# Kernel tuning notes

Measured on AMD Instinct MI355X. Metric: run time of the kernel, lower is better.

## Reference

```python
import jax, jax.numpy as jnp
import numpy as np

B, C, E = 2, 1024, 1024
H = 16            # n_heads as declared (used as per-group feature dim due to module's reshape)
HD = E // H       # 64 — the axis actually batched over in attention


def setup_inputs() -> dict:
    key = jax.random.key(0)
    ks = jax.random.split(key, 5)
    scale = 0.02
    return {
        "x": jax.random.normal(ks[0], (B, C, E), dtype=jnp.float32),
        "W_q": jax.random.normal(ks[1], (E, E), dtype=jnp.float32) * scale,
        "W_k": jax.random.normal(ks[2], (E, E), dtype=jnp.float32) * scale,
        "W_v": jax.random.normal(ks[3], (E, E), dtype=jnp.float32) * scale,
        "W_o": jax.random.normal(ks[4], (E, E), dtype=jnp.float32) * scale,
    }


def reference(x, W_q, W_k, W_v, W_o):
    # nn.Linear: y = x @ W.T  (bias=False)
    def proj_split(W):
        y = jnp.einsum('bce,de->bcd', x, W)              # [B,C,E]
        # view(B, C, HD, H).transpose(1,2) -> [B, HD, C, H]  (faithful to source layout)
        return y.reshape(B, C, HD, H).transpose(0, 2, 1, 3)

    Q = proj_split(W_q)
    K = proj_split(W_k)
    V = proj_split(W_v)

    scale = 1.0 / jnp.sqrt(jnp.asarray(H, dtype=x.dtype))  # sqrt of last dim (= n_heads here)
    scores = jnp.einsum('bdqh,bdkh->bdqk', Q, K) * scale    # [B, HD, C, C]
    weights = jax.nn.softmax(scores, axis=-1)
    out = jnp.einsum('bdqk,bdkh->bdqh', weights, V)         # [B, HD, C, H]
    out = out.transpose(0, 2, 1, 3).reshape(B, C, E)        # [B, C, E]
    out = jnp.einsum('bce,de->bcd', out, W_o)
    return out  # dropout p=0.0 / eval mode: identity
```

## Files before the change

kernel.cpp:

```cpp
#include <hip/hip_runtime.h>
#include <stdint.h>
#include <math.h>


typedef __bf16   bf16x8 __attribute__((ext_vector_type(8)));
typedef float    f32x4  __attribute__((ext_vector_type(4)));

__device__ __forceinline__ unsigned short f2bf(float f) {
    unsigned int u = __float_as_uint(f);
    u += 0x7FFFu + ((u >> 16) & 1u);
    return (unsigned short)(u >> 16);
}

__device__ __forceinline__ unsigned int cvtpk(float lo, float hi) {
    unsigned int r;
    asm("v_cvt_pk_bf16_f32 %0, %1, %2" : "=v"(r) : "v"(lo), "v"(hi));
    return r;
}

__device__ __forceinline__ void gl16(const unsigned short* g, unsigned short* l) {
    __builtin_amdgcn_global_load_lds(
        (const __attribute__((address_space(1))) unsigned int*)g,
        (__attribute__((address_space(3))) unsigned int*)l, 16, 0, 0);
}

__global__ __launch_bounds__(256) void cast_to_bf16(
    const float* __restrict__ x,
    const float* __restrict__ w0, const float* __restrict__ w1,
    const float* __restrict__ w2, const float* __restrict__ w3,
    unsigned short* __restrict__ xb,
    unsigned short* __restrict__ b0, unsigned short* __restrict__ b1,
    unsigned short* __restrict__ b2, unsigned short* __restrict__ b3)
{
    const int z = blockIdx.y;
    const float* src;
    unsigned short* dst;
    size_t off = 0;
    float sc = 1.f;
    if (z < 2)       { src = x;  dst = xb; off = (size_t)z << 20; }
    else if (z == 2) { src = w0; dst = b0; sc = 0.36067376022224085f; }
    else if (z == 3) { src = w1; dst = b1; }
    else if (z == 4) { src = w2; dst = b2; }
    else             { src = w3; dst = b3; }
    const size_t i = off + ((size_t)blockIdx.x * 256 + threadIdx.x) * 4;
    const float4 v = *(const float4*)(src + i);
    *(ushort4*)(dst + i) = make_ushort4(f2bf(v.x * sc), f2bf(v.y * sc),
                                        f2bf(v.z * sc), f2bf(v.w * sc));
}

__global__ __launch_bounds__(256) void gemm128_bt_mfma(
    const unsigned short* __restrict__ A,
    const unsigned short* __restrict__ B0, const unsigned short* __restrict__ B1,
    const unsigned short* __restrict__ B2,
    unsigned short* __restrict__ C0, unsigned short* __restrict__ C1,
    unsigned short* __restrict__ C2,
    int M, int N, int K)
{
    const unsigned short* Bm = (blockIdx.z == 0) ? B0 : (blockIdx.z == 1) ? B1 : B2;
    unsigned short* Cm       = (blockIdx.z == 0) ? C0 : (blockIdx.z == 1) ? C1 : C2;

    __shared__ __align__(16) unsigned short As[2][128 * 32];
    __shared__ __align__(16) unsigned short Bs[2][128 * 32];

    const int t    = threadIdx.x;
    const int lane = t & 63;
    const int w    = t >> 6;
    const int m0   = blockIdx.y * 128;
    const int n0   = blockIdx.x * 128;
    const int wm   = (w & 1) * 64;
    const int wn   = (w >> 1) * 64;

    const int r0 = t >> 2;
    const int c0 = (t & 3) * 8;
    const unsigned short* Apa = A  + (size_t)(m0 + r0) * K + c0;
    const unsigned short* Apb = Apa + (size_t)64 * K;
    const unsigned short* Bpa = Bm + (size_t)(n0 + r0) * K + c0;
    const unsigned short* Bpb = Bpa + (size_t)64 * K;
    unsigned short* lA0 = &As[0][w * 512];
    unsigned short* lA1 = &As[0][2048 + w * 512];
    unsigned short* lB0 = &Bs[0][w * 512];
    unsigned short* lB1 = &Bs[0][2048 + w * 512];
    const int bufStr = 128 * 32;

    f32x4 acc[4][4];
#pragma unroll
    for (int i = 0; i < 4; ++i)
#pragma unroll
        for (int j = 0; j < 4; ++j) acc[i][j] = (f32x4){0.f, 0.f, 0.f, 0.f};

    const int fm = lane & 15;
    const int kg = lane >> 4;

    gl16(Apa, lA0);
    gl16(Apb, lA1);
    gl16(Bpa, lB0);
    gl16(Bpb, lB1);

    int cur = 0;
    for (int k0 = 0; k0 < K; k0 += 32) {
        __syncthreads();

        if (k0 + 32 < K) {
            const int nb = (cur ^ 1);
            gl16(Apa + k0 + 32, lA0 + nb * bufStr);
            gl16(Apb + k0 + 32, lA1 + nb * bufStr);
            gl16(Bpa + k0 + 32, lB0 + nb * bufStr);
            gl16(Bpb + k0 + 32, lB1 + nb * bufStr);
        }

        const unsigned short* Ab = &As[cur][0];
        const unsigned short* Bb = &Bs[cur][0];
        bf16x8 af[4], bfr[4];
#pragma unroll
        for (int im = 0; im < 4; ++im)
            af[im] = *(const bf16x8*)&Ab[(wm + im * 16 + fm) * 32 + kg * 8];
#pragma unroll
        for (int in = 0; in < 4; ++in)
            bfr[in] = *(const bf16x8*)&Bb[(wn + in * 16 + fm) * 32 + kg * 8];
#pragma unroll
        for (int im = 0; im < 4; ++im)
#pragma unroll
            for (int in = 0; in < 4; ++in)
                acc[im][in] = __builtin_amdgcn_mfma_f32_16x16x32_bf16(
                    af[im], bfr[in], acc[im][in], 0, 0, 0);

        cur ^= 1;
    }

#pragma unroll
    for (int im = 0; im < 4; ++im) {
#pragma unroll
        for (int in = 0; in < 4; ++in) {
            const int row = m0 + wm + im * 16 + kg * 4;
            const int col = n0 + wn + in * 16 + fm;
#pragma unroll
            for (int r = 0; r < 4; ++r)
                Cm[(size_t)(row + r) * N + col] = f2bf(acc[im][in][r]);
        }
    }
}

__global__ __launch_bounds__(256) void gemm_bt_mfma(
    const unsigned short* __restrict__ A,
    const unsigned short* __restrict__ B0, const unsigned short* __restrict__ B1,
    const unsigned short* __restrict__ B2,
    void* __restrict__ C0, void* __restrict__ C1, void* __restrict__ C2,
    int M, int N, int K, int bf16out)
{
    const unsigned short* Bm = (blockIdx.z == 0) ? B0 : (blockIdx.z == 1) ? B1 : B2;
    void* Cm                 = (blockIdx.z == 0) ? C0 : (blockIdx.z == 1) ? C1 : C2;

    __shared__ __align__(16) unsigned short As[2][64 * 32];
    __shared__ __align__(16) unsigned short Bs[2][128 * 32];

    const int t    = threadIdx.x;
    const int lane = t & 63;
    const int w    = t >> 6;
    const int m0   = blockIdx.y * 64;
    const int n0   = blockIdx.x * 128;
    const int wm   = (w & 1) * 32;
    const int wn   = (w >> 1) * 64;

    const int r0 = t >> 2;
    const int c0 = (t & 3) * 8;
    const unsigned short* Apa = A  + (size_t)(m0 + r0) * K + c0;
    const unsigned short* Bpa = Bm + (size_t)(n0 + r0) * K + c0;
    const unsigned short* Bpb = Bm + (size_t)(n0 + r0 + 64) * K + c0;
    unsigned short* ldsA  = &As[0][w * 512];
    unsigned short* ldsB0 = &Bs[0][w * 512];
    unsigned short* ldsB1 = &Bs[0][2048 + w * 512];
    const int bufStrA = 64 * 32;
    const int bufStrB = 128 * 32;

    f32x4 acc[2][4];
#pragma unroll
    for (int i = 0; i < 2; ++i)
#pragma unroll
        for (int j = 0; j < 4; ++j) acc[i][j] = (f32x4){0.f, 0.f, 0.f, 0.f};

    const int fm = lane & 15;
    const int kg = lane >> 4;

    gl16(Apa, ldsA);
    gl16(Bpa, ldsB0);
    gl16(Bpb, ldsB1);

    int cur = 0;
    for (int k0 = 0; k0 < K; k0 += 32) {
        __syncthreads();

        if (k0 + 32 < K) {
            const int nb = (cur ^ 1);
            gl16(Apa + k0 + 32, ldsA  + nb * bufStrA);
            gl16(Bpa + k0 + 32, ldsB0 + nb * bufStrB);
            gl16(Bpb + k0 + 32, ldsB1 + nb * bufStrB);
        }

        const unsigned short* Ab = &As[cur][0];
        const unsigned short* Bb = &Bs[cur][0];
        bf16x8 af[2], bfr[4];
#pragma unroll
        for (int im = 0; im < 2; ++im)
            af[im] = *(const bf16x8*)&Ab[(wm + im * 16 + fm) * 32 + kg * 8];
#pragma unroll
        for (int in = 0; in < 4; ++in)
            bfr[in] = *(const bf16x8*)&Bb[(wn + in * 16 + fm) * 32 + kg * 8];
#pragma unroll
        for (int im = 0; im < 2; ++im)
#pragma unroll
            for (int in = 0; in < 4; ++in)
                acc[im][in] = __builtin_amdgcn_mfma_f32_16x16x32_bf16(
                    af[im], bfr[in], acc[im][in], 0, 0, 0);

        cur ^= 1;
    }

#pragma unroll
    for (int im = 0; im < 2; ++im) {
#pragma unroll
        for (int in = 0; in < 4; ++in) {
            const int row = m0 + wm + im * 16 + kg * 4;
            const int col = n0 + wn + in * 16 + fm;
            if (bf16out) {
                unsigned short* cp = (unsigned short*)Cm;
#pragma unroll
                for (int r = 0; r < 4; ++r)
                    cp[(size_t)(row + r) * N + col] = f2bf(acc[im][in][r]);
            } else {
                float* cp = (float*)Cm;
#pragma unroll
                for (int r = 0; r < 4; ++r)
                    cp[(size_t)(row + r) * N + col] = acc[im][in][r];
            }
        }
    }
}

#define KSTR  40
#define VSTRD 136
#define PSTRD 136

__global__ __launch_bounds__(256, 3) void attn_mfma(
    const unsigned short* __restrict__ Qb, const unsigned short* __restrict__ Kb,
    const unsigned short* __restrict__ Vb, unsigned short* __restrict__ Ob)
{
    __shared__ __align__(16) unsigned char smem[49408];
    unsigned short* Ks  = (unsigned short*)smem;
    unsigned short* VsT = (unsigned short*)(smem + 10240);
    unsigned short* Ps  = (unsigned short*)(smem + 14592);
    float*          Red = (float*)smem;

    const int t    = threadIdx.x;
    const int lane = t & 63;
    const int wv   = t >> 6;
    const int fm   = lane & 15;
    const int kg   = lane >> 4;
    const int bh   = blockIdx.y;
    const size_t base = ((size_t)(bh >> 6) << 20) + (size_t)(bh & 63) * 16;
    const int q0 = blockIdx.x * 128;
    const int wk = wv * 32;

    {
        const int row = t >> 1, seg = t & 1;
        *(uint4*)&Ks[row * KSTR + 16 + seg * 8] = make_uint4(0, 0, 0, 0);
    }

    union { uint4 u; bf16x8 h; } zz; zz.u = make_uint4(0, 0, 0, 0);
    bf16x8 aq[8];
#pragma unroll
    for (int m = 0; m < 8; ++m) {
        if (kg < 2)
            aq[m] = *(const bf16x8*)(Qb + base +
                     (size_t)(q0 + m * 16 + fm) * 1024 + kg * 8);
        else
            aq[m] = zz.h;
    }

    f32x4 oacc[8];
    float lp[8];
#pragma unroll
    for (int m = 0; m < 8; ++m) {
        oacc[m] = (f32x4){0.f, 0.f, 0.f, 0.f};
        lp[m] = 0.f;
    }

    for (int kt = 0; kt < 1024; kt += 128) {
        __syncthreads();
        {
            const int row = t >> 1, seg = t & 1;
            *(uint4*)&Ks[row * KSTR + seg * 8] =
                *(const uint4*)(Kb + base + (size_t)(kt + row) * 1024 + seg * 8);
            uint4 v = *(const uint4*)(Vb + base + (size_t)(kt + row) * 1024 + seg * 8);
            const unsigned short* pv = (const unsigned short*)&v;
#pragma unroll
            for (int d = 0; d < 8; ++d)
                VsT[(seg * 8 + d) * VSTRD + row] = pv[d];
        }
        __syncthreads();

        const bf16x8 bk0 = *(const bf16x8*)&Ks[(wk + fm) * KSTR + kg * 8];
        const bf16x8 bk1 = *(const bf16x8*)&Ks[(wk + 16 + fm) * KSTR + kg * 8];

#pragma unroll
        for (int m = 0; m < 8; ++m) {
            f32x4 s0 = __builtin_amdgcn_mfma_f32_16x16x32_bf16(
                bk0, aq[m], (f32x4){0.f, 0.f, 0.f, 0.f}, 0, 0, 0);
            f32x4 s1 = __builtin_amdgcn_mfma_f32_16x16x32_bf16(
                bk1, aq[m], (f32x4){0.f, 0.f, 0.f, 0.f}, 0, 0, 0);
            const float p0 = __builtin_amdgcn_exp2f(s0[0]);
            const float p1 = __builtin_amdgcn_exp2f(s0[1]);
            const float p2 = __builtin_amdgcn_exp2f(s0[2]);
            const float p3 = __builtin_amdgcn_exp2f(s0[3]);
            const float p4 = __builtin_amdgcn_exp2f(s1[0]);
            const float p5 = __builtin_amdgcn_exp2f(s1[1]);
            const float p6 = __builtin_amdgcn_exp2f(s1[2]);
            const float p7 = __builtin_amdgcn_exp2f(s1[3]);
            lp[m] += ((p0 + p1) + (p2 + p3)) + ((p4 + p5) + (p6 + p7));
            unsigned short* prow = &Ps[(m * 16 + fm) * PSTRD + wk];
            *(uint2*)&prow[kg * 4]      = make_uint2(cvtpk(p0, p1), cvtpk(p2, p3));
            *(uint2*)&prow[16 + kg * 4] = make_uint2(cvtpk(p4, p5), cvtpk(p6, p7));
        }

        const bf16x8 bv = *(const bf16x8*)&VsT[fm * VSTRD + wk + kg * 8];
#pragma unroll
        for (int m = 0; m < 8; ++m) {
            const bf16x8 ap = *(const bf16x8*)&Ps[(m * 16 + fm) * PSTRD + wk + kg * 8];
            oacc[m] = __builtin_amdgcn_mfma_f32_16x16x32_bf16(ap, bv, oacc[m], 0, 0, 0);
        }
    }

#pragma unroll
    for (int m = 0; m < 8; ++m) {
        lp[m] += __shfl_xor(lp[m], 16, 64);
        lp[m] += __shfl_xor(lp[m], 32, 64);
    }

    __syncthreads();
#pragma unroll
    for (int m = 0; m < 8; ++m) {
#pragma unroll
        for (int r = 0; r < 4; ++r)
            Red[((wv * 128) + m * 16 + kg * 4 + r) * 17 + fm] = oacc[m][r];
        if (kg == 0)
            Red[((wv * 128) + m * 16 + fm) * 17 + 16] = lp[m];
    }
    __syncthreads();

#pragma unroll
    for (int mp = 0; mp < 2; ++mp) {
#pragma unroll
        for (int r = 0; r < 4; ++r) {
            const int q = wv * 32 + mp * 16 + kg * 4 + r;
            const float o = Red[q * 17 + fm]         + Red[(128 + q) * 17 + fm] +
                            Red[(256 + q) * 17 + fm] + Red[(384 + q) * 17 + fm];
            const float l = Red[q * 17 + 16]         + Red[(128 + q) * 17 + 16] +
                            Red[(256 + q) * 17 + 16] + Red[(384 + q) * 17 + 16];
            Ob[base + (size_t)(q0 + q) * 1024 + fm] = f2bf(o / l);
        }
    }
}

extern "C" void kernel_launch(void* const* d_in, const int* in_sizes, int n_in,
                              void* d_out, int out_size, void* d_ws, size_t ws_size,
                              hipStream_t stream) {
    const float* x  = (const float*)d_in[0];
    const float* Wq = (const float*)d_in[1];
    const float* Wk = (const float*)d_in[2];
    const float* Wv = (const float*)d_in[3];
    const float* Wo = (const float*)d_in[4];
    float* out = (float*)d_out;

    const int M = 2048, N = 1024, Kd = 1024;
    const size_t MEG = 1048576;
    unsigned short* ws = (unsigned short*)d_ws;
    unsigned short* xb  = ws;
    unsigned short* Wqb = ws + 2 * MEG;
    unsigned short* Wkb = ws + 3 * MEG;
    unsigned short* Wvb = ws + 4 * MEG;
    unsigned short* Wob = ws + 5 * MEG;
    unsigned short* Qb  = ws + 6 * MEG;
    unsigned short* Kb  = ws + 8 * MEG;
    unsigned short* Vb  = ws + 10 * MEG;
    unsigned short* Ob  = ws + 12 * MEG;

    dim3 gc(1024, 6, 1);
    cast_to_bf16<<<gc, 256, 0, stream>>>(x, Wq, Wk, Wv, Wo, xb, Wqb, Wkb, Wvb, Wob);

    dim3 g1(N / 128, M / 128, 3);
    gemm128_bt_mfma<<<g1, 256, 0, stream>>>(xb, Wqb, Wkb, Wvb, Qb, Kb, Vb, M, N, Kd);

    dim3 g2(8, 128, 1);
    attn_mfma<<<g2, 256, 0, stream>>>(Qb, Kb, Vb, Ob);

    dim3 g3(N / 128, M / 64, 1);
    gemm_bt_mfma<<<g3, 256, 0, stream>>>(Ob, Wob, Wob, Wob, out, out, out, M, N, Kd, 0);
}
```

Measured before the change: 153.3 us.

## Fuse all stages into one persistent kernel with atomic grid barriers

Replaces the four separate launches (cast, QKV GEMM, attention, output GEMM) with a single persistent kernel of 512 blocks. Each block loops over the work tiles of every stage, and a spin-wait atomic grid barrier separates the stages. The aim is to remove launch gaps and inter-kernel drain/fill overhead. In exchange, the attention stage drops from occupancy 3 to launch bounds of 2, and tiles are distributed unevenly per block (384 and 256 tiles over 512 blocks leave some idle). A memset is added to reset the barrier counters, and correctness depends on all 512 blocks being co-resident.

After: 298.3 us. +94.6%, slower.

```diff
diff --git a/kernel.cpp b/kernel.cpp
--- a/kernel.cpp
+++ b/kernel.cpp
@@ -5,6 +5,8 @@
 
 typedef __bf16   bf16x8 __attribute__((ext_vector_type(8)));
 typedef float    f32x4  __attribute__((ext_vector_type(4)));
+
+#define NBLK 512
 
 __device__ __forceinline__ unsigned short f2bf(float f) {
     unsigned int u = __float_as_uint(f);
@@ -24,49 +26,36 @@
         (__attribute__((address_space(3))) unsigned int*)l, 16, 0, 0);
 }
 
-__global__ __launch_bounds__(256) void cast_to_bf16(
-    const float* __restrict__ x,
-    const float* __restrict__ w0, const float* __restrict__ w1,
-    const float* __restrict__ w2, const float* __restrict__ w3,
-    unsigned short* __restrict__ xb,
-    unsigned short* __restrict__ b0, unsigned short* __restrict__ b1,
-    unsigned short* __restrict__ b2, unsigned short* __restrict__ b3)
+__device__ __forceinline__ void gridbar(unsigned int* cnt) {
+    __syncthreads();
+    if (threadIdx.x == 0) {
+        __threadfence();
+        atomicAdd(cnt, 1u);
+        while (__hip_atomic_load(cnt, __ATOMIC_RELAXED,
+                                 __HIP_MEMORY_SCOPE_AGENT) < NBLK)
+            __builtin_amdgcn_s_sleep(4);
+        __threadfence();
+    }
+    __syncthreads();
+}
+
+__device__ void dev_gemm128(int bx, int by, int bz, unsigned char* smem,
+    const unsigned short* A,
+    const unsigned short* B0, const unsigned short* B1, const unsigned short* B2,
+    unsigned short* C0, unsigned short* C1, unsigned short* C2)
 {
-    const int z = blockIdx.y;
-    const float* src;
-    unsigned short* dst;
-    size_t off = 0;
-    float sc = 1.f;
-    if (z < 2)       { src = x;  dst = xb; off = (size_t)z << 20; }
-    else if (z == 2) { src = w0; dst = b0; sc = 0.36067376022224085f; }
-    else if (z == 3) { src = w1; dst = b1; }
-    else if (z == 4) { src = w2; dst = b2; }
-    else             { src = w3; dst = b3; }
-    const size_t i = off + ((size_t)blockIdx.x * 256 + threadIdx.x) * 4;
-    const float4 v = *(const float4*)(src + i);
-    *(ushort4*)(dst + i) = make_ushort4(f2bf(v.x * sc), f2bf(v.y * sc),
-                                        f2bf(v.z * sc), f2bf(v.w * sc));
-}
-
-__global__ __launch_bounds__(256) void gemm128_bt_mfma(
-    const unsigned short* __restrict__ A,
-    const unsigned short* __restrict__ B0, const unsigned short* __restrict__ B1,
-    const unsigned short* __restrict__ B2,
-    unsigned short* __restrict__ C0, unsigned short* __restrict__ C1,
-    unsigned short* __restrict__ C2,
-    int M, int N, int K)
-{
-    const unsigned short* Bm = (blockIdx.z == 0) ? B0 : (blockIdx.z == 1) ? B1 : B2;
-    unsigned short* Cm       = (blockIdx.z == 0) ? C0 : (blockIdx.z == 1) ? C1 : C2;
-
-    __shared__ __align__(16) unsigned short As[2][128 * 32];
-    __shared__ __align__(16) unsigned short Bs[2][128 * 32];
+    const int K = 1024, N = 1024;
+    const unsigned short* Bm = (bz == 0) ? B0 : (bz == 1) ? B1 : B2;
+    unsigned short* Cm       = (bz == 0) ? C0 : (bz == 1) ? C1 : C2;
+
+    unsigned short* As = (unsigned short*)smem;
+    unsigned short* Bs = (unsigned short*)(smem + 16384);
 
     const int t    = threadIdx.x;
     const int lane = t & 63;
     const int w    = t >> 6;
-    const int m0   = blockIdx.y * 128;
-    const int n0   = blockIdx.x * 128;
+    const int m0   = by * 128;
+    const int n0   = bx * 128;
     const int wm   = (w & 1) * 64;
     const int wn   = (w >> 1) * 64;
 
@@ -76,10 +65,10 @@
     const unsigned short* Apb = Apa + (size_t)64 * K;
     const unsigned short* Bpa = Bm + (size_t)(n0 + r0) * K + c0;
     const unsigned short* Bpb = Bpa + (size_t)64 * K;
-    unsigned short* lA0 = &As[0][w * 512];
-    unsigned short* lA1 = &As[0][2048 + w * 512];
-    unsigned short* lB0 = &Bs[0][w * 512];
-    unsigned short* lB1 = &Bs[0][2048 + w * 512];
+    unsigned short* lA0 = As + w * 512;
+    unsigned short* lA1 = As + 2048 + w * 512;
+    unsigned short* lB0 = Bs + w * 512;
+    unsigned short* lB1 = Bs + 2048 + w * 512;
     const int bufStr = 128 * 32;
 
     f32x4 acc[4][4];
@@ -108,8 +97,8 @@
             gl16(Bpb + k0 + 32, lB1 + nb * bufStr);
         }
 
-        const unsigned short* Ab = &As[cur][0];
-        const unsigned short* Bb = &Bs[cur][0];
+        const unsigned short* Ab = As + cur * bufStr;
+        const unsigned short* Bb = Bs + cur * bufStr;
         bf16x8 af[4], bfr[4];
 #pragma unroll
         for (int im = 0; im < 4; ++im)
@@ -140,24 +129,18 @@
     }
 }
 
-__global__ __launch_bounds__(256) void gemm_bt_mfma(
-    const unsigned short* __restrict__ A,
-    const unsigned short* __restrict__ B0, const unsigned short* __restrict__ B1,
-    const unsigned short* __restrict__ B2,
-    void* __restrict__ C0, void* __restrict__ C1, void* __restrict__ C2,
-    int M, int N, int K, int bf16out)
+__device__ void dev_gemm64(int bx, int by, unsigned char* smem,
+    const unsigned short* A, const unsigned short* Bm, float* Cm)
 {
-    const unsigned short* Bm = (blockIdx.z == 0) ? B0 : (blockIdx.z == 1) ? B1 : B2;
-    void* Cm                 = (blockIdx.z == 0) ? C0 : (blockIdx.z == 1) ? C1 : C2;
-
-    __shared__ __align__(16) unsigned short As[2][64 * 32];
-    __shared__ __align__(16) unsigned short Bs[2][128 * 32];
+    const int K = 1024, N = 1024;
+    unsigned short* As = (unsigned short*)smem;
+    unsigned short* Bs = (unsigned short*)(smem + 8192);
 
     const int t    = threadIdx.x;
     const int lane = t & 63;
     const int w    = t >> 6;
-    const int m0   = blockIdx.y * 64;
-    const int n0   = blockIdx.x * 128;
+    const int m0   = by * 64;
+    const int n0   = bx * 128;
     const int wm   = (w & 1) * 32;
     const int wn   = (w >> 1) * 64;
 
@@ -166,9 +149,9 @@
     const unsigned short* Apa = A  + (size_t)(m0 + r0) * K + c0;
     const unsigned short* Bpa = Bm + (size_t)(n0 + r0) * K + c0;
     const unsigned short* Bpb = Bm + (size_t)(n0 + r0 + 64) * K + c0;
-    unsigned short* ldsA  = &As[0][w * 512];
-    unsigned short* ldsB0 = &Bs[0][w * 512];
-    unsigned short* ldsB1 = &Bs[0][2048 + w * 512];
+    unsigned short* ldsA  = As + w * 512;
+    unsigned short* ldsB0 = Bs + w * 512;
+    unsigned short* ldsB1 = Bs + 2048 + w * 512;
     const int bufStrA = 64 * 32;
     const int bufStrB = 128 * 32;
 
@@ -196,8 +179,8 @@
             gl16(Bpb + k0 + 32, ldsB1 + nb * bufStrB);
         }
 
-        const unsigned short* Ab = &As[cur][0];
-        const unsigned short* Bb = &Bs[cur][0];
+        const unsigned short* Ab = As + cur * bufStrA;
+        const unsigned short* Bb = Bs + cur * bufStrB;
         bf16x8 af[2], bfr[4];
 #pragma unroll
         for (int im = 0; im < 2; ++im)
@@ -221,17 +204,9 @@
         for (int in = 0; in < 4; ++in) {
             const int row = m0 + wm + im * 16 + kg * 4;
             const int col = n0 + wn + in * 16 + fm;
-            if (bf16out) {
-                unsigned short* cp = (unsigned short*)Cm;
-#pragma unroll
-                for (int r = 0; r < 4; ++r)
-                    cp[(size_t)(row + r) * N + col] = f2bf(acc[im][in][r]);
-            } else {
-                float* cp = (float*)Cm;
-#pragma unroll
-                for (int r = 0; r < 4; ++r)
-                    cp[(size_t)(row + r) * N + col] = acc[im][in][r];
-            }
+#pragma unroll
+            for (int r = 0; r < 4; ++r)
+                Cm[(size_t)(row + r) * N + col] = acc[im][in][r];
         }
     }
 }
@@ -240,11 +215,10 @@
 #define VSTRD 136
 #define PSTRD 136
 
-__global__ __launch_bounds__(256, 3) void attn_mfma(
-    const unsigned short* __restrict__ Qb, const unsigned short* __restrict__ Kb,
-    const unsigned short* __restrict__ Vb, unsigned short* __restrict__ Ob)
+__device__ void dev_attn(int bx, int by, unsigned char* smem,
+    const unsigned short* Qb, const unsigned short* Kb,
+    const unsigned short* Vb, unsigned short* Ob)
 {
-    __shared__ __align__(16) unsigned char smem[49408];
     unsigned short* Ks  = (unsigned short*)smem;
     unsigned short* VsT = (unsigned short*)(smem + 10240);
     unsigned short* Ps  = (unsigned short*)(smem + 14592);
@@ -255,10 +229,11 @@
     const int wv   = t >> 6;
     const int fm   = lane & 15;
     const int kg   = lane >> 4;
-    const int bh   = blockIdx.y;
-    const size_t base = ((size_t)(bh >> 6) << 20) + (size_t)(bh & 63) * 16;
-    const int q0 = blockIdx.x * 128;
+    const size_t base = ((size_t)(by >> 6) << 20) + (size_t)(by & 63) * 16;
+    const int q0 = bx * 128;
     const int wk = wv * 32;
+
+    __syncthreads();
 
     {
         const int row = t >> 1, seg = t & 1;
@@ -360,6 +335,58 @@
     }
 }
 
+__global__ __launch_bounds__(256, 2) void fused_mha(
+    const float* __restrict__ x,
+    const float* __restrict__ Wq, const float* __restrict__ Wk,
+    const float* __restrict__ Wv, const float* __restrict__ Wo,
+    unsigned short* ws16, float* out, unsigned int* bars)
+{
+    __shared__ __align__(16) unsigned char smem[49408];
+    const int t   = threadIdx.x;
+    const int blk = blockIdx.x;
+
+    const size_t MEG = 1048576;
+    unsigned short* xb  = ws16;
+    unsigned short* Wqb = ws16 + 2 * MEG;
+    unsigned short* Wkb = ws16 + 3 * MEG;
+    unsigned short* Wvb = ws16 + 4 * MEG;
+    unsigned short* Wob = ws16 + 5 * MEG;
+    unsigned short* Qb  = ws16 + 6 * MEG;
+    unsigned short* Kb  = ws16 + 8 * MEG;
+    unsigned short* Vb  = ws16 + 10 * MEG;
+    unsigned short* Ob  = ws16 + 12 * MEG;
+
+    for (int j = blk; j < 6144; j += NBLK) {
+        const int z = j >> 10;
+        const float* src;
+        unsigned short* dst;
+        size_t off = 0;
+        float sc = 1.f;
+        if (z < 2)       { src = x;  dst = xb; off = (size_t)z << 20; }
+        else if (z == 2) { src = Wq; dst = Wqb; sc = 0.36067376022224085f; }
+        else if (z == 3) { src = Wk; dst = Wkb; }
+        else if (z == 4) { src = Wv; dst = Wvb; }
+        else             { src = Wo; dst = Wob; }
+        const size_t i = off + ((size_t)(j & 1023) * 256 + t) * 4;
+        const float4 v = *(const float4*)(src + i);
+        *(ushort4*)(dst + i) = make_ushort4(f2bf(v.x * sc), f2bf(v.y * sc),
+                                            f2bf(v.z * sc), f2bf(v.w * sc));
+    }
+    gridbar(bars + 0);
+
+    for (int j = blk; j < 384; j += NBLK)
+        dev_gemm128(j & 7, (j >> 3) & 15, j >> 7, smem,
+                    xb, Wqb, Wkb, Wvb, Qb, Kb, Vb);
+    gridbar(bars + 1);
+
+    for (int j = blk; j < 1024; j += NBLK)
+        dev_attn(j & 7, j >> 3, smem, Qb, Kb, Vb, Ob);
+    gridbar(bars + 2);
+
+    for (int j = blk; j < 256; j += NBLK)
+        dev_gemm64(j & 7, j >> 3, smem, Ob, Wob, out);
+}
+
 extern "C" void kernel_launch(void* const* d_in, const int* in_sizes, int n_in,
                               void* d_out, int out_size, void* d_ws, size_t ws_size,
                               hipStream_t stream) {
@@ -370,28 +397,10 @@
     const float* Wo = (const float*)d_in[4];
     float* out = (float*)d_out;
 
-    const int M = 2048, N = 1024, Kd = 1024;
     const size_t MEG = 1048576;
     unsigned short* ws = (unsigned short*)d_ws;
-    unsigned short* xb  = ws;
-    unsigned short* Wqb = ws + 2 * MEG;
-    unsigned short* Wkb = ws + 3 * MEG;
-    unsigned short* Wvb = ws + 4 * MEG;
-    unsigned short* Wob = ws + 5 * MEG;
-    unsigned short* Qb  = ws + 6 * MEG;
-    unsigned short* Kb  = ws + 8 * MEG;
-    unsigned short* Vb  = ws + 10 * MEG;
-    unsigned short* Ob  = ws + 12 * MEG;
-
-    dim3 gc(1024, 6, 1);
-    cast_to_bf16<<<gc, 256, 0, stream>>>(x, Wq, Wk, Wv, Wo, xb, Wqb, Wkb, Wvb, Wob);
-
-    dim3 g1(N / 128, M / 128, 3);
-    gemm128_bt_mfma<<<g1, 256, 0, stream>>>(xb, Wqb, Wkb, Wvb, Qb, Kb, Vb, M, N, Kd);
-
-    dim3 g2(8, 128, 1);
-    attn_mfma<<<g2, 256, 0, stream>>>(Qb, Kb, Vb, Ob);
-
-    dim3 g3(N / 128, M / 64, 1);
-    gemm_bt_mfma<<<g3, 256, 0, stream>>>(Ob, Wob, Wob, Wob, out, out, out, M, N, Kd, 0);
-}
+    unsigned int* bars = (unsigned int*)(ws + 24 * MEG);
+
+    hipMemsetAsync(bars, 0, 64, stream);
+    fused_mha<<<dim3(NBLK), dim3(256), 0, stream>>>(x, Wq, Wk, Wv, Wo, ws, out, bars);
+}
```

## Make attention waves independent with per-wave LDS slices and no block barriers

Applied to the files above, without the earlier changes.

Each wave now stages only its own 32-key slice of V and its own P tile in private LDS regions, and loads K fragments straight from global memory into registers. This removes both per-iteration block-wide __syncthreads and shrinks shared memory, with launch bounds raised to allow 4 blocks per CU. The cost is that K is read redundantly from global per wave. The unpadded P stride of 32 may also cause LDS bank conflicts.

New measurement: 162.5 us. +6.0%, slower.

```diff
diff --git a/kernel.cpp b/kernel.cpp
--- a/kernel.cpp
+++ b/kernel.cpp
@@ -236,19 +236,14 @@
     }
 }
 
-#define KSTR  40
-#define VSTRD 136
-#define PSTRD 136
-
-__global__ __launch_bounds__(256, 3) void attn_mfma(
+#define VSTRW 40
+#define PSTRW 32
+
+__global__ __launch_bounds__(256, 4) void attn_mfma(
     const unsigned short* __restrict__ Qb, const unsigned short* __restrict__ Kb,
     const unsigned short* __restrict__ Vb, unsigned short* __restrict__ Ob)
 {
-    __shared__ __align__(16) unsigned char smem[49408];
-    unsigned short* Ks  = (unsigned short*)smem;
-    unsigned short* VsT = (unsigned short*)(smem + 10240);
-    unsigned short* Ps  = (unsigned short*)(smem + 14592);
-    float*          Red = (float*)smem;
+    __shared__ __align__(16) unsigned char smem[37888];
 
     const int t    = threadIdx.x;
     const int lane = t & 63;
@@ -260,10 +255,9 @@
     const int q0 = blockIdx.x * 128;
     const int wk = wv * 32;
 
-    {
-        const int row = t >> 1, seg = t & 1;
-        *(uint4*)&Ks[row * KSTR + 16 + seg * 8] = make_uint4(0, 0, 0, 0);
-    }
+    unsigned short* VsT = (unsigned short*)(smem + wv * 1280);
+    unsigned short* Ps  = (unsigned short*)(smem + 5120 + wv * 8192);
+    float*          Red = (float*)smem;
 
     union { uint4 u; bf16x8 h; } zz; zz.u = make_uint4(0, 0, 0, 0);
     bf16x8 aq[8];
@@ -285,21 +279,23 @@
     }
 
     for (int kt = 0; kt < 1024; kt += 128) {
-        __syncthreads();
         {
-            const int row = t >> 1, seg = t & 1;
-            *(uint4*)&Ks[row * KSTR + seg * 8] =
-                *(const uint4*)(Kb + base + (size_t)(kt + row) * 1024 + seg * 8);
-            uint4 v = *(const uint4*)(Vb + base + (size_t)(kt + row) * 1024 + seg * 8);
+            const int key = lane >> 1, half = lane & 1;
+            const uint4 v = *(const uint4*)(Vb + base +
+                             (size_t)(kt + wk + key) * 1024 + half * 8);
             const unsigned short* pv = (const unsigned short*)&v;
 #pragma unroll
             for (int d = 0; d < 8; ++d)
-                VsT[(seg * 8 + d) * VSTRD + row] = pv[d];
-        }
-        __syncthreads();
-
-        const bf16x8 bk0 = *(const bf16x8*)&Ks[(wk + fm) * KSTR + kg * 8];
-        const bf16x8 bk1 = *(const bf16x8*)&Ks[(wk + 16 + fm) * KSTR + kg * 8];
+                VsT[(half * 8 + d) * VSTRW + key] = pv[d];
+        }
+
+        bf16x8 bk0 = zz.h, bk1 = zz.h;
+        if (kg < 2) {
+            bk0 = *(const bf16x8*)(Kb + base +
+                   (size_t)(kt + wk + fm) * 1024 + kg * 8);
+            bk1 = *(const bf16x8*)(Kb + base +
+                   (size_t)(kt + wk + 16 + fm) * 1024 + kg * 8);
+        }
 
 #pragma unroll
         for (int m = 0; m < 8; ++m) {
@@ -316,15 +312,15 @@
             const float p6 = __builtin_amdgcn_exp2f(s1[2]);
             const float p7 = __builtin_amdgcn_exp2f(s1[3]);
             lp[m] += ((p0 + p1) + (p2 + p3)) + ((p4 + p5) + (p6 + p7));
-            unsigned short* prow = &Ps[(m * 16 + fm) * PSTRD + wk];
+            unsigned short* prow = Ps + (m * 16 + fm) * PSTRW;
             *(uint2*)&prow[kg * 4]      = make_uint2(cvtpk(p0, p1), cvtpk(p2, p3));
             *(uint2*)&prow[16 + kg * 4] = make_uint2(cvtpk(p4, p5), cvtpk(p6, p7));
         }
 
-        const bf16x8 bv = *(const bf16x8*)&VsT[fm * VSTRD + wk + kg * 8];
+        const bf16x8 bv = *(const bf16x8*)&VsT[fm * VSTRW + kg * 8];
 #pragma unroll
         for (int m = 0; m < 8; ++m) {
-            const bf16x8 ap = *(const bf16x8*)&Ps[(m * 16 + fm) * PSTRD + wk + kg * 8];
+            const bf16x8 ap = *(const bf16x8*)&Ps[(m * 16 + fm) * PSTRW + kg * 8];
             oacc[m] = __builtin_amdgcn_mfma_f32_16x16x32_bf16(ap, bv, oacc[m], 0, 0, 0);
         }
     }
```
